# Kernel optimization log

Hardware: AMD Instinct MI355X
Metric: run time of the kernel (lower is better)

## Reference

```python
import jax, jax.numpy as jnp
import numpy as np

EPS = 1e-12  # F.normalize default eps


def setup_inputs() -> dict:
    key = jax.random.key(0)
    ks = jax.random.split(key, 8)
    B, T, D, S = 512, 256, 256, 8
    inputs = jax.random.normal(ks[0], (B, T, D), dtype=jnp.float32)
    lengths = jax.random.randint(ks[1], (B,), 1, T + 1, dtype=jnp.int32)
    keys = jax.random.uniform(ks[2], (S, D), minval=-0.1, maxval=0.1, dtype=jnp.float32)
    xav = 1.0 / np.sqrt(D)  # xavier_normal std for square matrix
    U = jax.random.normal(ks[3], (D, D), dtype=jnp.float32) * xav
    V = jax.random.normal(ks[4], (D, D), dtype=jnp.float32) * xav
    W = jax.random.normal(ks[5], (D, D), dtype=jnp.float32) * xav
    gate_bias = jnp.zeros((1,), dtype=jnp.float32)
    state_bias = jnp.zeros((1, D), dtype=jnp.float32)
    return {"inputs": inputs, "lengths": lengths, "keys": keys, "U": U,
            "V": V, "W": W, "gate_bias": gate_bias, "state_bias": state_bias}


def reference(inputs, lengths, keys, U, V, W, gate_bias, state_bias):
    # inputs: [B, T, D]; keys: [S, D]; states carried as [B, S, D]
    B, T, D = inputs.shape
    S = keys.shape[0]
    keyV = keys @ V  # [S, D], loop-invariant
    init_states = jnp.broadcast_to(keys[None], (B, S, D))  # zero_state
    mask = (jnp.arange(T)[:, None] < lengths[None, :])  # [T, B]

    def step(states, xm):
        x, m = xm  # x: [B, D], m: [B]
        # gate: <x, state_j> + <x, key_j> + bias  -> [B, S]
        g = jax.nn.sigmoid(jnp.einsum('bd,bsd->bs', x, states)
                           + x @ keys.T + gate_bias)
        # candidate: state@U + key@V + x@W + state_bias -> [B, S, D]
        h_tilda = jax.nn.elu(jnp.einsum('bsd,de->bse', states, U)
                             + keyV[None]
                             + (x @ W)[:, None, :]
                             + state_bias[None])
        h = states + g[..., None] * h_tilda
        h = h / jnp.maximum(jnp.linalg.norm(h, axis=-1, keepdims=True), EPS)
        new_states = jnp.where(m[:, None, None], h, states)
        return new_states, None

    final_states, _ = jax.lax.scan(step, init_states,
                                   (jnp.swapaxes(inputs, 0, 1), mask))
    return final_states  # [B, S, D] == torch.stack(hiddens, dim=1)
```

## Files before the change

### kernel.cpp

```cpp
#include <hip/hip_runtime.h>
#include <math.h>

namespace {
constexpr int kB = 512;
constexpr int kT = 256;
constexpr int kD = 256;
constexpr int kS = 8;
constexpr int kStRow = 292;
constexpr int kRedRow = 12;

__device__ __forceinline__ int physk(int k) { return k + ((k >> 5) << 2); }
}

__global__ __launch_bounds__(256, 2)
void xw_gemm_kernel(const float* __restrict__ X, const float* __restrict__ W,
                    const int* __restrict__ lengths, float* __restrict__ XW) {
  const int m0 = blockIdx.x * 32;
  const int b = m0 >> 8;
  const int t0 = m0 & 255;
  if (t0 >= lengths[b]) return;

  __shared__ float Xs[32][kD];
  const int tid = threadIdx.x;
  const int j  = tid & 63;
  const int rg = tid >> 6;

  const float4* Xg4 = (const float4*)(X + (size_t)m0 * kD);
  float4* Xs4 = (float4*)&Xs[0][0];
  for (int i = tid; i < 32 * kD / 4; i += 256) Xs4[i] = Xg4[i];
  __syncthreads();

  float4 acc[8];
#pragma unroll
  for (int i = 0; i < 8; ++i) acc[i] = make_float4(0.f, 0.f, 0.f, 0.f);

  const float4* W4 = (const float4*)W;
  const float4* Xrow = (const float4*)&Xs[rg * 8][0];

  for (int k4 = 0; k4 < kD / 4; ++k4) {
    float4 w0 = W4[(size_t)(4 * k4 + 0) * 64 + j];
    float4 w1 = W4[(size_t)(4 * k4 + 1) * 64 + j];
    float4 w2 = W4[(size_t)(4 * k4 + 2) * 64 + j];
    float4 w3 = W4[(size_t)(4 * k4 + 3) * 64 + j];
#pragma unroll
    for (int i = 0; i < 8; ++i) {
      float4 x = Xrow[i * 64 + k4];
      acc[i].x = fmaf(x.x, w0.x, fmaf(x.y, w1.x, fmaf(x.z, w2.x, fmaf(x.w, w3.x, acc[i].x))));
      acc[i].y = fmaf(x.x, w0.y, fmaf(x.y, w1.y, fmaf(x.z, w2.y, fmaf(x.w, w3.y, acc[i].y))));
      acc[i].z = fmaf(x.x, w0.z, fmaf(x.y, w1.z, fmaf(x.z, w2.z, fmaf(x.w, w3.z, acc[i].z))));
      acc[i].w = fmaf(x.x, w0.w, fmaf(x.y, w1.w, fmaf(x.z, w2.w, fmaf(x.w, w3.w, acc[i].w))));
    }
  }
  float4* XW4 = (float4*)XW;
#pragma unroll
  for (int i = 0; i < 8; ++i)
    XW4[(size_t)(m0 + rg * 8 + i) * 64 + j] = acc[i];
}

__global__ __launch_bounds__(256, 4)
void gk_kernel(const float* __restrict__ inputs, const float* __restrict__ keys,
               const int* __restrict__ lengths, float* __restrict__ GK) {
  const int b = blockIdx.x;
  const int tid = threadIdx.x;
  const int lane = tid & 63;
  const int wid = tid >> 6;
  const int len = lengths[b];

  __shared__ float4 Ks4[kS * 64];
  for (int i = tid; i < kS * 64; i += 256) Ks4[i] = ((const float4*)keys)[i];
  __syncthreads();

  const float4* X4 = (const float4*)inputs;
  for (int t = wid; t < len; t += 4) {
    float4 x = X4[((size_t)b * kT + t) * 64 + lane];
    float p[kS];
#pragma unroll
    for (int s = 0; s < kS; ++s) {
      float4 kk = Ks4[s * 64 + lane];
      p[s] = fmaf(x.x, kk.x, fmaf(x.y, kk.y, fmaf(x.z, kk.z, x.w * kk.w)));
    }
#pragma unroll
    for (int off = 32; off >= 1; off >>= 1) {
#pragma unroll
      for (int s = 0; s < kS; ++s) p[s] += __shfl_xor(p[s], off, 64);
    }
    if (lane == 0) {
      float* g = GK + ((size_t)b * kT + t) * kS;
#pragma unroll
      for (int s = 0; s < kS; ++s) g[s] = p[s];
    }
  }
}

__global__ __launch_bounds__(512)
void sort_lengths_kernel(const int* __restrict__ lengths, int* __restrict__ order) {
  __shared__ int L[kB];
  const int i = threadIdx.x;
  L[i] = lengths[i];
  __syncthreads();
  const int li = L[i];
  int r = 0;
  for (int j = 0; j < kB; ++j) {
    const int lj = L[j];
    r += (lj > li || (lj == li && j < i)) ? 1 : 0;
  }
  order[r] = i;
}

__global__ __launch_bounds__(512, 2)
void dynmem_rec4_kernel(const float* __restrict__ inputs,
                        const int*   __restrict__ lengths,
                        const float* __restrict__ keys,
                        const float* __restrict__ U,
                        const float* __restrict__ V,
                        const float* __restrict__ gate_bias,
                        const float* __restrict__ state_bias,
                        const float* __restrict__ XW,
                        const float* __restrict__ GK,
                        const int*   __restrict__ order,
                        float* __restrict__ out)
{
  const int blk = blockIdx.x;
  const int bA = order[blk];
  const int bB = order[kB - 1 - blk];
  const int tid = threadIdx.x;
  const int w = tid >> 6;
  const int lane = tid & 63;
  const int q = lane & 7;
  const int jj = lane >> 3;
  const int cg = w * 8 + jj;
  const int c0 = 4 * cg;
  const int c0p = physk(c0);

  __shared__ float StA[kS * kStRow];
  __shared__ float StB[kS * kStRow];
  __shared__ float KVL[kS * kD];
  __shared__ float redGA[kS * kRedRow], redGB[kS * kRedRow];
  __shared__ float redNA[kS * kRedRow], redNB[kS * kRedRow];

  for (int i = tid; i < kS * kD; i += 512) {
    int s = i >> 8, dd = i & 255;
    float kv = keys[i];
    int pa = s * kStRow + physk(dd);
    StA[pa] = kv;
    StB[pa] = kv;
  }

  float4 u4[32];
#pragma unroll
  for (int kk = 0; kk < 32; ++kk)
    u4[kk] = *(const float4*)(U + (size_t)(q * 32 + kk) * kD + c0);

  {
    const int h2 = tid >> 8, d = tid & 255;
    float a0 = 0.f, a1 = 0.f, a2 = 0.f, a3 = 0.f;
    const float* Vc = V + d;
    const float* K0 = keys + (size_t)(4 * h2 + 0) * kD;
    const float* K1 = keys + (size_t)(4 * h2 + 1) * kD;
    const float* K2 = keys + (size_t)(4 * h2 + 2) * kD;
    const float* K3 = keys + (size_t)(4 * h2 + 3) * kD;
    for (int k = 0; k < kD; ++k) {
      float v = Vc[(size_t)k * kD];
      a0 = fmaf(K0[k], v, a0);
      a1 = fmaf(K1[k], v, a1);
      a2 = fmaf(K2[k], v, a2);
      a3 = fmaf(K3[k], v, a3);
    }
    float sb = state_bias[d];
    KVL[(4 * h2 + 0) * kD + d] = a0 + sb;
    KVL[(4 * h2 + 1) * kD + d] = a1 + sb;
    KVL[(4 * h2 + 2) * kD + d] = a2 + sb;
    KVL[(4 * h2 + 3) * kD + d] = a3 + sb;
  }

  const float gb = gate_bias[0];
  int lenA = lengths[bA]; lenA = lenA < 0 ? 0 : (lenA > kT ? kT : lenA);
  int lenB = lengths[bB]; lenB = lenB < 0 ? 0 : (lenB > kT ? kT : lenB);
  const int lenM = lenA > lenB ? lenA : lenB;

  __syncthreads();

  const float4 kvq = *(const float4*)(KVL + q * kD + c0);
  float4 srA = *(const float4*)(StA + q * kStRow + c0p);
  float4 srB = *(const float4*)(StB + q * kStRow + c0p);

  const float* SqA = StA + q * 36;
  const float* SqB = StB + q * 36;

  for (int t = 0; t < lenM; ++t) {
    const bool dA = t < lenA;
    const bool dB = t < lenB;

    float4 xA4, xwA4, xB4, xwB4;
    float gkqA = 0.f, gkqB = 0.f;
    if (dA) {
      const size_t baseA = (size_t)bA * kT + t;
      xA4  = *(const float4*)(inputs + baseA * kD + c0);
      xwA4 = *(const float4*)(XW + baseA * kD + c0);
      gkqA = GK[baseA * kS + q];
    }
    if (dB) {
      const size_t baseB = (size_t)bB * kT + t;
      xB4  = *(const float4*)(inputs + baseB * kD + c0);
      xwB4 = *(const float4*)(XW + baseB * kD + c0);
      gkqB = GK[baseB * kS + q];
    }

    if (dA) {
      float pg = fmaf(xA4.x, srA.x, fmaf(xA4.y, srA.y, fmaf(xA4.z, srA.z, xA4.w * srA.w)));
      pg += __shfl_xor(pg, 8, 64);
      pg += __shfl_xor(pg, 16, 64);
      pg += __shfl_xor(pg, 32, 64);
      if (lane < 8) redGA[lane * kRedRow + w] = pg;
    }
    if (dB) {
      float pg = fmaf(xB4.x, srB.x, fmaf(xB4.y, srB.y, fmaf(xB4.z, srB.z, xB4.w * srB.w)));
      pg += __shfl_xor(pg, 8, 64);
      pg += __shfl_xor(pg, 16, 64);
      pg += __shfl_xor(pg, 32, 64);
      if (lane < 8) redGB[lane * kRedRow + w] = pg;
    }

    float4 cA = make_float4(0.f, 0.f, 0.f, 0.f);
    if (dA) {
      float4 C[8];
#pragma unroll
      for (int s = 0; s < 8; ++s) C[s] = make_float4(0.f, 0.f, 0.f, 0.f);
#pragma unroll
      for (int k4 = 0; k4 < 8; ++k4) {
        const float4 u0 = u4[4 * k4 + 0], u1 = u4[4 * k4 + 1];
        const float4 u2 = u4[4 * k4 + 2], u3 = u4[4 * k4 + 3];
#pragma unroll
        for (int s = 0; s < 8; ++s) {
          float4 sv = *(const float4*)(SqA + s * kStRow + 4 * k4);
          C[s].x = fmaf(sv.x, u0.x, fmaf(sv.y, u1.x, fmaf(sv.z, u2.x, fmaf(sv.w, u3.x, C[s].x))));
          C[s].y = fmaf(sv.x, u0.y, fmaf(sv.y, u1.y, fmaf(sv.z, u2.y, fmaf(sv.w, u3.y, C[s].y))));
          C[s].z = fmaf(sv.x, u0.z, fmaf(sv.y, u1.z, fmaf(sv.z, u2.z, fmaf(sv.w, u3.z, C[s].z))));
          C[s].w = fmaf(sv.x, u0.w, fmaf(sv.y, u1.w, fmaf(sv.z, u2.w, fmaf(sv.w, u3.w, C[s].w))));
        }
      }
#pragma unroll
      for (int off = 1; off <= 4; off <<= 1) {
#pragma unroll
        for (int s = 0; s < 8; ++s) {
          C[s].x += __shfl_xor(C[s].x, off, 64);
          C[s].y += __shfl_xor(C[s].y, off, 64);
          C[s].z += __shfl_xor(C[s].z, off, 64);
          C[s].w += __shfl_xor(C[s].w, off, 64);
        }
      }
      cA = C[0];
#pragma unroll
      for (int s = 1; s < 8; ++s) {
        if (q == s) cA = C[s];
      }
    }

    float4 cB = make_float4(0.f, 0.f, 0.f, 0.f);
    if (dB) {
      float4 C[8];
#pragma unroll
      for (int s = 0; s < 8; ++s) C[s] = make_float4(0.f, 0.f, 0.f, 0.f);
#pragma unroll
      for (int k4 = 0; k4 < 8; ++k4) {
        const float4 u0 = u4[4 * k4 + 0], u1 = u4[4 * k4 + 1];
        const float4 u2 = u4[4 * k4 + 2], u3 = u4[4 * k4 + 3];
#pragma unroll
        for (int s = 0; s < 8; ++s) {
          float4 sv = *(const float4*)(SqB + s * kStRow + 4 * k4);
          C[s].x = fmaf(sv.x, u0.x, fmaf(sv.y, u1.x, fmaf(sv.z, u2.x, fmaf(sv.w, u3.x, C[s].x))));
          C[s].y = fmaf(sv.x, u0.y, fmaf(sv.y, u1.y, fmaf(sv.z, u2.y, fmaf(sv.w, u3.y, C[s].y))));
          C[s].z = fmaf(sv.x, u0.z, fmaf(sv.y, u1.z, fmaf(sv.z, u2.z, fmaf(sv.w, u3.z, C[s].z))));
          C[s].w = fmaf(sv.x, u0.w, fmaf(sv.y, u1.w, fmaf(sv.z, u2.w, fmaf(sv.w, u3.w, C[s].w))));
        }
      }
#pragma unroll
      for (int off = 1; off <= 4; off <<= 1) {
#pragma unroll
        for (int s = 0; s < 8; ++s) {
          C[s].x += __shfl_xor(C[s].x, off, 64);
          C[s].y += __shfl_xor(C[s].y, off, 64);
          C[s].z += __shfl_xor(C[s].z, off, 64);
          C[s].w += __shfl_xor(C[s].w, off, 64);
        }
      }
      cB = C[0];
#pragma unroll
      for (int s = 1; s < 8; ++s) {
        if (q == s) cB = C[s];
      }
    }

    __syncthreads();

    float4 hA, hB;
    if (dA) {
      float4 ra = *(const float4*)(redGA + q * kRedRow);
      float4 rb = *(const float4*)(redGA + q * kRedRow + 4);
      float gs = ((ra.x + ra.y) + (ra.z + ra.w)) + ((rb.x + rb.y) + (rb.z + rb.w)) + gkqA + gb;
      float gq = 1.f / (1.f + expf(-gs));
      float t0 = cA.x + kvq.x + xwA4.x; t0 = t0 > 0.f ? t0 : expm1f(t0);
      float t1 = cA.y + kvq.y + xwA4.y; t1 = t1 > 0.f ? t1 : expm1f(t1);
      float t2 = cA.z + kvq.z + xwA4.z; t2 = t2 > 0.f ? t2 : expm1f(t2);
      float t3 = cA.w + kvq.w + xwA4.w; t3 = t3 > 0.f ? t3 : expm1f(t3);
      hA.x = fmaf(gq, t0, srA.x);
      hA.y = fmaf(gq, t1, srA.y);
      hA.z = fmaf(gq, t2, srA.z);
      hA.w = fmaf(gq, t3, srA.w);
      float pn = fmaf(hA.x, hA.x, fmaf(hA.y, hA.y, fmaf(hA.z, hA.z, hA.w * hA.w)));
      pn += __shfl_xor(pn, 8, 64);
      pn += __shfl_xor(pn, 16, 64);
      pn += __shfl_xor(pn, 32, 64);
      if (lane < 8) redNA[lane * kRedRow + w] = pn;
    }
    if (dB) {
      float4 ra = *(const float4*)(redGB + q * kRedRow);
      float4 rb = *(const float4*)(redGB + q * kRedRow + 4);
      float gs = ((ra.x + ra.y) + (ra.z + ra.w)) + ((rb.x + rb.y) + (rb.z + rb.w)) + gkqB + gb;
      float gq = 1.f / (1.f + expf(-gs));
      float t0 = cB.x + kvq.x + xwB4.x; t0 = t0 > 0.f ? t0 : expm1f(t0);
      float t1 = cB.y + kvq.y + xwB4.y; t1 = t1 > 0.f ? t1 : expm1f(t1);
      float t2 = cB.z + kvq.z + xwB4.z; t2 = t2 > 0.f ? t2 : expm1f(t2);
      float t3 = cB.w + kvq.w + xwB4.w; t3 = t3 > 0.f ? t3 : expm1f(t3);
      hB.x = fmaf(gq, t0, srB.x);
      hB.y = fmaf(gq, t1, srB.y);
      hB.z = fmaf(gq, t2, srB.z);
      hB.w = fmaf(gq, t3, srB.w);
      float pn = fmaf(hB.x, hB.x, fmaf(hB.y, hB.y, fmaf(hB.z, hB.z, hB.w * hB.w)));
      pn += __shfl_xor(pn, 8, 64);
      pn += __shfl_xor(pn, 16, 64);
      pn += __shfl_xor(pn, 32, 64);
      if (lane < 8) redNB[lane * kRedRow + w] = pn;
    }
    __syncthreads();

    if (dA) {
      float4 na = *(const float4*)(redNA + q * kRedRow);
      float4 nb = *(const float4*)(redNA + q * kRedRow + 4);
      float ns = ((na.x + na.y) + (na.z + na.w)) + ((nb.x + nb.y) + (nb.z + nb.w));
      float inh = 1.f / fmaxf(sqrtf(ns), 1e-12f);
      srA.x = hA.x * inh; srA.y = hA.y * inh; srA.z = hA.z * inh; srA.w = hA.w * inh;
      *(float4*)(StA + q * kStRow + c0p) = srA;
    }
    if (dB) {
      float4 na = *(const float4*)(redNB + q * kRedRow);
      float4 nb = *(const float4*)(redNB + q * kRedRow + 4);
      float ns = ((na.x + na.y) + (na.z + na.w)) + ((nb.x + nb.y) + (nb.z + nb.w));
      float inh = 1.f / fmaxf(sqrtf(ns), 1e-12f);
      srB.x = hB.x * inh; srB.y = hB.y * inh; srB.z = hB.z * inh; srB.w = hB.w * inh;
      *(float4*)(StB + q * kStRow + c0p) = srB;
    }
    __syncthreads();
  }

  for (int i = tid; i < kS * kD; i += 512) {
    int s = i >> 8, dd = i & 255;
    int pa = s * kStRow + physk(dd);
    out[(size_t)bA * kS * kD + i] = StA[pa];
    out[(size_t)bB * kS * kD + i] = StB[pa];
  }
}

extern "C" void kernel_launch(void* const* d_in, const int* in_sizes, int n_in,
                              void* d_out, int out_size, void* d_ws, size_t ws_size,
                              hipStream_t stream) {
  const float* inputs     = (const float*)d_in[0];
  const int*   lengths    = (const int*)  d_in[1];
  const float* keys       = (const float*)d_in[2];
  const float* U          = (const float*)d_in[3];
  const float* V          = (const float*)d_in[4];
  const float* W          = (const float*)d_in[5];
  const float* gate_bias  = (const float*)d_in[6];
  const float* state_bias = (const float*)d_in[7];

  const size_t xw_elems = (size_t)kB * kT * kD;
  const size_t gk_elems = (size_t)kB * kT * kS;
  float* XW = (float*)d_ws;
  float* GK = (float*)d_ws + xw_elems;
  int*   order = (int*)((float*)d_ws + xw_elems + gk_elems);

  sort_lengths_kernel<<<dim3(1), dim3(512), 0, stream>>>(lengths, order);
  xw_gemm_kernel<<<dim3((kB * kT) / 32), dim3(256), 0, stream>>>(inputs, W, lengths, XW);
  gk_kernel<<<dim3(kB), dim3(256), 0, stream>>>(inputs, keys, lengths, GK);
  dynmem_rec4_kernel<<<dim3(kB / 2), dim3(512), 0, stream>>>(
      inputs, lengths, keys, U, V, gate_bias, state_bias, XW, GK, order, (float*)d_out);
}
```

Measured before the change: 2.395 ms.

## Split recurrence over 1024 threads with 16-way K split and DPP reductions

The recurrent kernel moves from 512 to 1024 threads per block. Each lane now holds 16 rows of U instead of 32, which halves per-thread FMA work and register pressure per timestep. The cross-lane K reduction uses DPP row operations instead of shuffles. The loop is bounded by lenA, relying on the length sort so that lenA >= lenB, and the XW/GK loads move later so they overlap the matvec. The risks are more barrier participants, duplicated work in lanes with q>=8, and one block per CU instead of two.

After: 4.951 ms. 2.07x slower.

```diff
diff --git a/kernel.cpp b/kernel.cpp
--- a/kernel.cpp
+++ b/kernel.cpp
@@ -7,9 +7,24 @@
 constexpr int kD = 256;
 constexpr int kS = 8;
 constexpr int kStRow = 292;
-constexpr int kRedRow = 12;
+constexpr int kRedRow = 20;
 
 __device__ __forceinline__ int physk(int k) { return k + ((k >> 5) << 2); }
+
+template <int CTRL>
+__device__ __forceinline__ float dpp_add(float v) {
+  int p = __builtin_amdgcn_update_dpp(0, __float_as_int(v), CTRL, 0xF, 0xF, false);
+  return v + __int_as_float(p);
+}
+template <int CTRL>
+__device__ __forceinline__ float4 dpp_add4(float4 v) {
+  float4 r;
+  r.x = dpp_add<CTRL>(v.x);
+  r.y = dpp_add<CTRL>(v.y);
+  r.z = dpp_add<CTRL>(v.z);
+  r.w = dpp_add<CTRL>(v.w);
+  return r;
+}
 }
 
 __global__ __launch_bounds__(256, 2)
@@ -107,8 +122,8 @@
   order[r] = i;
 }
 
-__global__ __launch_bounds__(512, 2)
-void dynmem_rec4_kernel(const float* __restrict__ inputs,
+__global__ __launch_bounds__(1024)
+void dynmem_rec5_kernel(const float* __restrict__ inputs,
                         const int*   __restrict__ lengths,
                         const float* __restrict__ keys,
                         const float* __restrict__ U,
@@ -126,11 +141,12 @@
   const int tid = threadIdx.x;
   const int w = tid >> 6;
   const int lane = tid & 63;
-  const int q = lane & 7;
-  const int jj = lane >> 3;
-  const int cg = w * 8 + jj;
+  const int q = lane & 15;
+  const int jj = lane >> 4;
+  const int cg = w * 4 + jj;
   const int c0 = 4 * cg;
   const int c0p = physk(c0);
+  const int s8 = q & 7;
 
   __shared__ float StA[kS * kStRow];
   __shared__ float StB[kS * kStRow];
@@ -138,7 +154,7 @@
   __shared__ float redGA[kS * kRedRow], redGB[kS * kRedRow];
   __shared__ float redNA[kS * kRedRow], redNB[kS * kRedRow];
 
-  for (int i = tid; i < kS * kD; i += 512) {
+  for (int i = tid; i < kS * kD; i += 1024) {
     int s = i >> 8, dd = i & 255;
     float kv = keys[i];
     int pa = s * kStRow + physk(dd);
@@ -146,93 +162,72 @@
     StB[pa] = kv;
   }
 
-  float4 u4[32];
-#pragma unroll
-  for (int kk = 0; kk < 32; ++kk)
-    u4[kk] = *(const float4*)(U + (size_t)(q * 32 + kk) * kD + c0);
+  float4 u4[16];
+  const int kbase = 16 * q;
+#pragma unroll
+  for (int kk = 0; kk < 16; ++kk)
+    u4[kk] = *(const float4*)(U + (size_t)(kbase + kk) * kD + c0);
 
   {
-    const int h2 = tid >> 8, d = tid & 255;
-    float a0 = 0.f, a1 = 0.f, a2 = 0.f, a3 = 0.f;
+    const int h4 = tid >> 8, d = tid & 255;
+    float a0 = 0.f, a1 = 0.f;
     const float* Vc = V + d;
-    const float* K0 = keys + (size_t)(4 * h2 + 0) * kD;
-    const float* K1 = keys + (size_t)(4 * h2 + 1) * kD;
-    const float* K2 = keys + (size_t)(4 * h2 + 2) * kD;
-    const float* K3 = keys + (size_t)(4 * h2 + 3) * kD;
+    const float* K0 = keys + (size_t)h4 * kD;
+    const float* K1 = keys + (size_t)(h4 + 4) * kD;
     for (int k = 0; k < kD; ++k) {
       float v = Vc[(size_t)k * kD];
       a0 = fmaf(K0[k], v, a0);
       a1 = fmaf(K1[k], v, a1);
-      a2 = fmaf(K2[k], v, a2);
-      a3 = fmaf(K3[k], v, a3);
     }
     float sb = state_bias[d];
-    KVL[(4 * h2 + 0) * kD + d] = a0 + sb;
-    KVL[(4 * h2 + 1) * kD + d] = a1 + sb;
-    KVL[(4 * h2 + 2) * kD + d] = a2 + sb;
-    KVL[(4 * h2 + 3) * kD + d] = a3 + sb;
+    KVL[h4 * kD + d] = a0 + sb;
+    KVL[(h4 + 4) * kD + d] = a1 + sb;
   }
 
   const float gb = gate_bias[0];
   int lenA = lengths[bA]; lenA = lenA < 0 ? 0 : (lenA > kT ? kT : lenA);
   int lenB = lengths[bB]; lenB = lenB < 0 ? 0 : (lenB > kT ? kT : lenB);
-  const int lenM = lenA > lenB ? lenA : lenB;
 
   __syncthreads();
 
-  const float4 kvq = *(const float4*)(KVL + q * kD + c0);
-  float4 srA = *(const float4*)(StA + q * kStRow + c0p);
-  float4 srB = *(const float4*)(StB + q * kStRow + c0p);
-
-  const float* SqA = StA + q * 36;
-  const float* SqB = StB + q * 36;
-
-  for (int t = 0; t < lenM; ++t) {
-    const bool dA = t < lenA;
+  float4 srA = *(const float4*)(StA + s8 * kStRow + c0p);
+  float4 srB = *(const float4*)(StB + s8 * kStRow + c0p);
+  const float* SA = StA + physk(kbase);
+  const float* SB = StB + physk(kbase);
+
+  for (int t = 0; t < lenA; ++t) {
     const bool dB = t < lenB;
-
-    float4 xA4, xwA4, xB4, xwB4;
-    float gkqA = 0.f, gkqB = 0.f;
-    if (dA) {
-      const size_t baseA = (size_t)bA * kT + t;
-      xA4  = *(const float4*)(inputs + baseA * kD + c0);
-      xwA4 = *(const float4*)(XW + baseA * kD + c0);
-      gkqA = GK[baseA * kS + q];
-    }
-    if (dB) {
-      const size_t baseB = (size_t)bB * kT + t;
-      xB4  = *(const float4*)(inputs + baseB * kD + c0);
-      xwB4 = *(const float4*)(XW + baseB * kD + c0);
-      gkqB = GK[baseB * kS + q];
-    }
-
-    if (dA) {
-      float pg = fmaf(xA4.x, srA.x, fmaf(xA4.y, srA.y, fmaf(xA4.z, srA.z, xA4.w * srA.w)));
-      pg += __shfl_xor(pg, 8, 64);
+    const size_t baseA = ((size_t)bA * kT + t) * (size_t)kD;
+    const size_t baseB = ((size_t)bB * kT + t) * (size_t)kD;
+
+    {
+      float4 xA = *(const float4*)(inputs + baseA + c0);
+      float pg = fmaf(xA.x, srA.x, fmaf(xA.y, srA.y, fmaf(xA.z, srA.z, xA.w * srA.w)));
       pg += __shfl_xor(pg, 16, 64);
       pg += __shfl_xor(pg, 32, 64);
       if (lane < 8) redGA[lane * kRedRow + w] = pg;
     }
     if (dB) {
-      float pg = fmaf(xB4.x, srB.x, fmaf(xB4.y, srB.y, fmaf(xB4.z, srB.z, xB4.w * srB.w)));
-      pg += __shfl_xor(pg, 8, 64);
+      float4 xB = *(const float4*)(inputs + baseB + c0);
+      float pg = fmaf(xB.x, srB.x, fmaf(xB.y, srB.y, fmaf(xB.z, srB.z, xB.w * srB.w)));
       pg += __shfl_xor(pg, 16, 64);
       pg += __shfl_xor(pg, 32, 64);
       if (lane < 8) redGB[lane * kRedRow + w] = pg;
     }
 
     float4 cA = make_float4(0.f, 0.f, 0.f, 0.f);
-    if (dA) {
+    float4 cB = make_float4(0.f, 0.f, 0.f, 0.f);
+    {
       float4 C[8];
 #pragma unroll
       for (int s = 0; s < 8; ++s) C[s] = make_float4(0.f, 0.f, 0.f, 0.f);
 #pragma unroll
-      for (int k4 = 0; k4 < 8; ++k4) {
+      for (int k4 = 0; k4 < 4; ++k4) {
         const float4 u0 = u4[4 * k4 + 0], u1 = u4[4 * k4 + 1];
         const float4 u2 = u4[4 * k4 + 2], u3 = u4[4 * k4 + 3];
 #pragma unroll
         for (int s = 0; s < 8; ++s) {
-          float4 sv = *(const float4*)(SqA + s * kStRow + 4 * k4);
+          float4 sv = *(const float4*)(SA + s * kStRow + 4 * k4);
           C[s].x = fmaf(sv.x, u0.x, fmaf(sv.y, u1.x, fmaf(sv.z, u2.x, fmaf(sv.w, u3.x, C[s].x))));
           C[s].y = fmaf(sv.x, u0.y, fmaf(sv.y, u1.y, fmaf(sv.z, u2.y, fmaf(sv.w, u3.y, C[s].y))));
           C[s].z = fmaf(sv.x, u0.z, fmaf(sv.y, u1.z, fmaf(sv.z, u2.z, fmaf(sv.w, u3.z, C[s].z))));
@@ -240,34 +235,30 @@
         }
       }
 #pragma unroll
-      for (int off = 1; off <= 4; off <<= 1) {
-#pragma unroll
-        for (int s = 0; s < 8; ++s) {
-          C[s].x += __shfl_xor(C[s].x, off, 64);
-          C[s].y += __shfl_xor(C[s].y, off, 64);
-          C[s].z += __shfl_xor(C[s].z, off, 64);
-          C[s].w += __shfl_xor(C[s].w, off, 64);
-        }
+      for (int s = 0; s < 8; ++s) {
+        C[s] = dpp_add4<0xB1>(C[s]);
+        C[s] = dpp_add4<0x4E>(C[s]);
+        C[s] = dpp_add4<0x141>(C[s]);
+        C[s] = dpp_add4<0x140>(C[s]);
       }
       cA = C[0];
 #pragma unroll
       for (int s = 1; s < 8; ++s) {
-        if (q == s) cA = C[s];
-      }
-    }
-
-    float4 cB = make_float4(0.f, 0.f, 0.f, 0.f);
+        if (s8 == s) cA = C[s];
+      }
+    }
+
     if (dB) {
       float4 C[8];
 #pragma unroll
       for (int s = 0; s < 8; ++s) C[s] = make_float4(0.f, 0.f, 0.f, 0.f);
 #pragma unroll
-      for (int k4 = 0; k4 < 8; ++k4) {
+      for (int k4 = 0; k4 < 4; ++k4) {
         const float4 u0 = u4[4 * k4 + 0], u1 = u4[4 * k4 + 1];
         const float4 u2 = u4[4 * k4 + 2], u3 = u4[4 * k4 + 3];
 #pragma unroll
         for (int s = 0; s < 8; ++s) {
-          float4 sv = *(const float4*)(SqB + s * kStRow + 4 * k4);
+          float4 sv = *(const float4*)(SB + s * kStRow + 4 * k4);
           C[s].x = fmaf(sv.x, u0.x, fmaf(sv.y, u1.x, fmaf(sv.z, u2.x, fmaf(sv.w, u3.x, C[s].x))));
           C[s].y = fmaf(sv.x, u0.y, fmaf(sv.y, u1.y, fmaf(sv.z, u2.y, fmaf(sv.w, u3.y, C[s].y))));
           C[s].z = fmaf(sv.x, u0.z, fmaf(sv.y, u1.z, fmaf(sv.z, u2.z, fmaf(sv.w, u3.z, C[s].z))));
@@ -275,85 +266,109 @@
         }
       }
 #pragma unroll
-      for (int off = 1; off <= 4; off <<= 1) {
-#pragma unroll
-        for (int s = 0; s < 8; ++s) {
-          C[s].x += __shfl_xor(C[s].x, off, 64);
-          C[s].y += __shfl_xor(C[s].y, off, 64);
-          C[s].z += __shfl_xor(C[s].z, off, 64);
-          C[s].w += __shfl_xor(C[s].w, off, 64);
-        }
+      for (int s = 0; s < 8; ++s) {
+        C[s] = dpp_add4<0xB1>(C[s]);
+        C[s] = dpp_add4<0x4E>(C[s]);
+        C[s] = dpp_add4<0x141>(C[s]);
+        C[s] = dpp_add4<0x140>(C[s]);
       }
       cB = C[0];
 #pragma unroll
       for (int s = 1; s < 8; ++s) {
-        if (q == s) cB = C[s];
-      }
+        if (s8 == s) cB = C[s];
+      }
+    }
+
+    const float4 xwA = *(const float4*)(XW + baseA + c0);
+    const float gkA = GK[((size_t)bA * kT + t) * kS + s8];
+    float4 xwB = make_float4(0.f, 0.f, 0.f, 0.f);
+    float gkB = 0.f;
+    if (dB) {
+      xwB = *(const float4*)(XW + baseB + c0);
+      gkB = GK[((size_t)bB * kT + t) * kS + s8];
     }
 
     __syncthreads();
 
-    float4 hA, hB;
-    if (dA) {
-      float4 ra = *(const float4*)(redGA + q * kRedRow);
-      float4 rb = *(const float4*)(redGA + q * kRedRow + 4);
-      float gs = ((ra.x + ra.y) + (ra.z + ra.w)) + ((rb.x + rb.y) + (rb.z + rb.w)) + gkqA + gb;
-      float gq = 1.f / (1.f + expf(-gs));
-      float t0 = cA.x + kvq.x + xwA4.x; t0 = t0 > 0.f ? t0 : expm1f(t0);
-      float t1 = cA.y + kvq.y + xwA4.y; t1 = t1 > 0.f ? t1 : expm1f(t1);
-      float t2 = cA.z + kvq.z + xwA4.z; t2 = t2 > 0.f ? t2 : expm1f(t2);
-      float t3 = cA.w + kvq.w + xwA4.w; t3 = t3 > 0.f ? t3 : expm1f(t3);
-      hA.x = fmaf(gq, t0, srA.x);
-      hA.y = fmaf(gq, t1, srA.y);
-      hA.z = fmaf(gq, t2, srA.z);
-      hA.w = fmaf(gq, t3, srA.w);
+    const float4 kvq = *(const float4*)(KVL + s8 * kD + c0);
+    float4 hA = make_float4(0.f, 0.f, 0.f, 0.f);
+    float4 hB = make_float4(0.f, 0.f, 0.f, 0.f);
+    {
+      const float* rg = redGA + s8 * kRedRow;
+      float4 ra = *(const float4*)(rg);
+      float4 rb = *(const float4*)(rg + 4);
+      float4 rc = *(const float4*)(rg + 8);
+      float4 rd = *(const float4*)(rg + 12);
+      float gs = (((ra.x + ra.y) + (ra.z + ra.w)) + ((rb.x + rb.y) + (rb.z + rb.w))) +
+                 (((rc.x + rc.y) + (rc.z + rc.w)) + ((rd.x + rd.y) + (rd.z + rd.w))) +
+                 gkA + gb;
+      float g = 1.f / (1.f + expf(-gs));
+      float t0 = cA.x + kvq.x + xwA.x; t0 = t0 > 0.f ? t0 : expm1f(t0);
+      float t1 = cA.y + kvq.y + xwA.y; t1 = t1 > 0.f ? t1 : expm1f(t1);
+      float t2 = cA.z + kvq.z + xwA.z; t2 = t2 > 0.f ? t2 : expm1f(t2);
+      float t3 = cA.w + kvq.w + xwA.w; t3 = t3 > 0.f ? t3 : expm1f(t3);
+      hA.x = fmaf(g, t0, srA.x);
+      hA.y = fmaf(g, t1, srA.y);
+      hA.z = fmaf(g, t2, srA.z);
+      hA.w = fmaf(g, t3, srA.w);
       float pn = fmaf(hA.x, hA.x, fmaf(hA.y, hA.y, fmaf(hA.z, hA.z, hA.w * hA.w)));
-      pn += __shfl_xor(pn, 8, 64);
       pn += __shfl_xor(pn, 16, 64);
       pn += __shfl_xor(pn, 32, 64);
       if (lane < 8) redNA[lane * kRedRow + w] = pn;
     }
     if (dB) {
-      float4 ra = *(const float4*)(redGB + q * kRedRow);
-      float4 rb = *(const float4*)(redGB + q * kRedRow + 4);
-      float gs = ((ra.x + ra.y) + (ra.z + ra.w)) + ((rb.x + rb.y) + (rb.z + rb.w)) + gkqB + gb;
-      float gq = 1.f / (1.f + expf(-gs));
-      float t0 = cB.x + kvq.x + xwB4.x; t0 = t0 > 0.f ? t0 : expm1f(t0);
-      float t1 = cB.y + kvq.y + xwB4.y; t1 = t1 > 0.f ? t1 : expm1f(t1);
-      float t2 = cB.z + kvq.z + xwB4.z; t2 = t2 > 0.f ? t2 : expm1f(t2);
-      float t3 = cB.w + kvq.w + xwB4.w; t3 = t3 > 0.f ? t3 : expm1f(t3);
-      hB.x = fmaf(gq, t0, srB.x);
-      hB.y = fmaf(gq, t1, srB.y);
-      hB.z = fmaf(gq, t2, srB.z);
-      hB.w = fmaf(gq, t3, srB.w);
+      const float* rg = redGB + s8 * kRedRow;
+      float4 ra = *(const float4*)(rg);
+      float4 rb = *(const float4*)(rg + 4);
+      float4 rc = *(const float4*)(rg + 8);
+      float4 rd = *(const float4*)(rg + 12);
+      float gs = (((ra.x + ra.y) + (ra.z + ra.w)) + ((rb.x + rb.y) + (rb.z + rb.w))) +
+                 (((rc.x + rc.y) + (rc.z + rc.w)) + ((rd.x + rd.y) + (rd.z + rd.w))) +
+                 gkB + gb;
+      float g = 1.f / (1.f + expf(-gs));
+      float t0 = cB.x + kvq.x + xwB.x; t0 = t0 > 0.f ? t0 : expm1f(t0);
+      float t1 = cB.y + kvq.y + xwB.y; t1 = t1 > 0.f ? t1 : expm1f(t1);
+      float t2 = cB.z + kvq.z + xwB.z; t2 = t2 > 0.f ? t2 : expm1f(t2);
+      float t3 = cB.w + kvq.w + xwB.w; t3 = t3 > 0.f ? t3 : expm1f(t3);
+      hB.x = fmaf(g, t0, srB.x);
+      hB.y = fmaf(g, t1, srB.y);
+      hB.z = fmaf(g, t2, srB.z);
+      hB.w = fmaf(g, t3, srB.w);
       float pn = fmaf(hB.x, hB.x, fmaf(hB.y, hB.y, fmaf(hB.z, hB.z, hB.w * hB.w)));
-      pn += __shfl_xor(pn, 8, 64);
       pn += __shfl_xor(pn, 16, 64);
       pn += __shfl_xor(pn, 32, 64);
       if (lane < 8) redNB[lane * kRedRow + w] = pn;
     }
     __syncthreads();
 
-    if (dA) {
-      float4 na = *(const float4*)(redNA + q * kRedRow);
-      float4 nb = *(const float4*)(redNA + q * kRedRow + 4);
-      float ns = ((na.x + na.y) + (na.z + na.w)) + ((nb.x + nb.y) + (nb.z + nb.w));
+    {
+      const float* rn = redNA + s8 * kRedRow;
+      float4 na = *(const float4*)(rn);
+      float4 nb = *(const float4*)(rn + 4);
+      float4 nc = *(const float4*)(rn + 8);
+      float4 nd = *(const float4*)(rn + 12);
+      float ns = (((na.x + na.y) + (na.z + na.w)) + ((nb.x + nb.y) + (nb.z + nb.w))) +
+                 (((nc.x + nc.y) + (nc.z + nc.w)) + ((nd.x + nd.y) + (nd.z + nd.w)));
       float inh = 1.f / fmaxf(sqrtf(ns), 1e-12f);
       srA.x = hA.x * inh; srA.y = hA.y * inh; srA.z = hA.z * inh; srA.w = hA.w * inh;
-      *(float4*)(StA + q * kStRow + c0p) = srA;
+      if (q < 8) *(float4*)(StA + s8 * kStRow + c0p) = srA;
     }
     if (dB) {
-      float4 na = *(const float4*)(redNB + q * kRedRow);
-      float4 nb = *(const float4*)(redNB + q * kRedRow + 4);
-      float ns = ((na.x + na.y) + (na.z + na.w)) + ((nb.x + nb.y) + (nb.z + nb.w));
+      const float* rn = redNB + s8 * kRedRow;
+      float4 na = *(const float4*)(rn);
+      float4 nb = *(const float4*)(rn + 4);
+      float4 nc = *(const float4*)(rn + 8);
+      float4 nd = *(const float4*)(rn + 12);
+      float ns = (((na.x + na.y) + (na.z + na.w)) + ((nb.x + nb.y) + (nb.z + nb.w))) +
+                 (((nc.x + nc.y) + (nc.z + nc.w)) + ((nd.x + nd.y) + (nd.z + nd.w)));
       float inh = 1.f / fmaxf(sqrtf(ns), 1e-12f);
       srB.x = hB.x * inh; srB.y = hB.y * inh; srB.z = hB.z * inh; srB.w = hB.w * inh;
-      *(float4*)(StB + q * kStRow + c0p) = srB;
+      if (q < 8) *(float4*)(StB + s8 * kStRow + c0p) = srB;
     }
     __syncthreads();
   }
 
-  for (int i = tid; i < kS * kD; i += 512) {
+  for (int i = tid; i < kS * kD; i += 1024) {
     int s = i >> 8, dd = i & 255;
     int pa = s * kStRow + physk(dd);
     out[(size_t)bA * kS * kD + i] = StA[pa];
@@ -382,6 +397,6 @@
   sort_lengths_kernel<<<dim3(1), dim3(512), 0, stream>>>(lengths, order);
   xw_gemm_kernel<<<dim3((kB * kT) / 32), dim3(256), 0, stream>>>(inputs, W, lengths, XW);
   gk_kernel<<<dim3(kB), dim3(256), 0, stream>>>(inputs, keys, lengths, GK);
-  dynmem_rec4_kernel<<<dim3(kB / 2), dim3(512), 0, stream>>>(
+  dynmem_rec5_kernel<<<dim3(kB / 2), dim3(1024), 0, stream>>>(
       inputs, lengths, keys, U, V, gate_bias, state_bias, XW, GK, order, (float*)d_out);
 }
```
